# Optimization experiments

Measured on AMD Instinct MI355X. Metric: run time of the kernel, lower is better.

The kernel has to match this reference:

```python
import jax, jax.numpy as jnp
import numpy as np

N = 100000
E = 6400000
IN_CH = 128
HID = 8
HEADS = 2
OUT_CH = 1
NEG_SLOPE = 0.2


def gat_conv(x, src, dst, W, a_src, a_dst, bias, heads, out_ch, concat, n_nodes):
    # x: [N, F_in], W: [F_in, heads*out_ch], a_src/a_dst: [heads, out_ch]
    h = (x @ W).reshape(n_nodes, heads, out_ch)          # [N, H, C]
    alpha_s = jnp.sum(h * a_src[None], axis=-1)          # [N, H]
    alpha_d = jnp.sum(h * a_dst[None], axis=-1)          # [N, H]
    alpha = alpha_s[src] + alpha_d[dst]                  # [E, H]
    alpha = jax.nn.leaky_relu(alpha, NEG_SLOPE)
    # segment softmax over incoming edges of each destination node
    seg_max = jax.ops.segment_max(alpha, dst, num_segments=n_nodes)  # [N, H]
    alpha = jnp.exp(alpha - seg_max[dst])
    denom = jax.ops.segment_sum(alpha, dst, num_segments=n_nodes)    # [N, H]
    alpha = alpha / (denom[dst] + 1e-16)
    msg = h[src] * alpha[..., None]                       # [E, H, C]
    out = jax.ops.segment_sum(msg, dst, num_segments=n_nodes)        # [N, H, C]
    if concat:
        out = out.reshape(n_nodes, heads * out_ch)
    else:
        out = out.mean(axis=1)
    return out + bias


def setup_inputs() -> dict:
    key = jax.random.key(0)
    ks = jax.random.split(key, 12)
    x = jax.random.normal(ks[0], (N, IN_CH), dtype=jnp.float32)
    edge_index = jax.random.randint(ks[1], (2, E), 0, N, dtype=jnp.int64)
    s1 = 1.0 / np.sqrt(IN_CH)
    W1 = jax.random.normal(ks[2], (IN_CH, HEADS * HID), dtype=jnp.float32) * s1
    a_src1 = jax.random.normal(ks[3], (HEADS, HID), dtype=jnp.float32) * (1.0 / np.sqrt(HID))
    a_dst1 = jax.random.normal(ks[4], (HEADS, HID), dtype=jnp.float32) * (1.0 / np.sqrt(HID))
    b1 = jnp.zeros((HEADS * HID,), dtype=jnp.float32)
    s2 = 1.0 / np.sqrt(HEADS * HID)
    W2 = jax.random.normal(ks[5], (HEADS * HID, OUT_CH), dtype=jnp.float32) * s2
    a_src2 = jax.random.normal(ks[6], (1, OUT_CH), dtype=jnp.float32)
    a_dst2 = jax.random.normal(ks[7], (1, OUT_CH), dtype=jnp.float32)
    b2 = jnp.zeros((OUT_CH,), dtype=jnp.float32)
    return {"x": x, "edge_index": edge_index, "W1": W1, "a_src1": a_src1,
            "a_dst1": a_dst1, "b1": b1, "W2": W2, "a_src2": a_src2,
            "a_dst2": a_dst2, "b2": b2}


def reference(x, edge_index, W1, a_src1, a_dst1, b1, W2, a_src2, a_dst2, b2):
    # add self-loops (PyG GATConv default)
    loops = jnp.arange(N, dtype=edge_index.dtype)
    src = jnp.concatenate([edge_index[0], loops])
    dst = jnp.concatenate([edge_index[1], loops])
    h = gat_conv(x, src, dst, W1, a_src1, a_dst1, b1, HEADS, HID, True, N)
    h = jax.nn.relu(h)
    out = gat_conv(h, src, dst, W2, a_src2, a_dst2, b2, 1, OUT_CH, False, N)
    return out
```

## Files before the change

kernel.cpp:

```cpp
#include <hip/hip_runtime.h>
#include <hip/hip_fp16.h>
#include <cstdint>
#include <cstddef>

#define N_NODES 100000
#define E_EDGES 6400000
#define E_TOT   (E_EDGES + N_NODES)
#define IN_CH   128
#define NHID    16
#define BSHIFT  8
#define BSZ     256
#define NBUCK   391
#define CHUNK   6144
#define BCAP    24
#define NCHUNK  ((E_TOT + CHUNK - 1) / CHUNK)
#define LCAP    18176

__global__ void k_detect(const int* __restrict__ edge, int* __restrict__ flag) {
    if (blockIdx.x == 0 && threadIdx.x == 0) {
        int odd_or = 0;
        for (int i = 0; i < 64; i++) odd_or |= edge[2 * i + 1];
        flag[0] = (odd_or == 0) ? 1 : 0;
    }
}

__global__ __launch_bounds__(256) void k_gemm1(
        const float* __restrict__ x, const float* __restrict__ W1,
        const float* __restrict__ a_src1, const float* __restrict__ a_dst1,
        __half* __restrict__ h16, float* __restrict__ asrc,
        float* __restrict__ adst) {
    __shared__ __align__(16) float sW[IN_CH * NHID];
    __shared__ __align__(16) float sx[16][132];
    __shared__ float sh[16][17];
    int t = threadIdx.x;
    int r = t >> 4, c = t & 15;
    int row = blockIdx.x * 16 + r;

    const float4* W4 = (const float4*)W1;
    ((float4*)sW)[t] = W4[t];
    ((float4*)sW)[t + 256] = W4[t + 256];

    if (row < N_NODES) {
        const float4* xr = (const float4*)(x + (size_t)row * IN_CH);
        float4 v0 = xr[c];
        float4 v1 = xr[c + 16];
        *(float4*)&sx[r][4 * c] = v0;
        *(float4*)&sx[r][64 + 4 * c] = v1;
    }
    __syncthreads();

    float acc = 0.f;
    if (row < N_NODES) {
        #pragma unroll 16
        for (int k = 0; k < IN_CH; k++) acc = fmaf(sx[r][k], sW[k * NHID + c], acc);
        h16[(size_t)row * NHID + c] = __float2half(acc);
    }
    sh[r][c] = acc;
    __syncthreads();

    if (row < N_NODES && c < 4) {
        int h = c & 1;
        const float* av = (c >= 2) ? a_dst1 : a_src1;
        float s = 0.f;
        #pragma unroll
        for (int q = 0; q < 8; q++) s = fmaf(sh[r][h * 8 + q], av[h * 8 + q], s);
        if (c < 2) asrc[2 * (size_t)row + c] = s;
        else       adst[2 * (size_t)row + (c - 2)] = s;
    }
}

__global__ __launch_bounds__(256) void k_ccount(const int* __restrict__ edge,
                                                const int* __restrict__ flag,
                                                int* __restrict__ ccnt) {
    __shared__ int sc[NBUCK];
    int m64 = flag[0];
    int t = threadIdx.x;
    for (int i = t; i < NBUCK; i += 256) sc[i] = 0;
    __syncthreads();
    size_t c0 = (size_t)blockIdx.x * CHUNK;
    size_t cend = c0 + CHUNK; if (cend > E_TOT) cend = E_TOT;
    size_t ee = (cend < (size_t)E_EDGES) ? cend : (size_t)E_EDGES;

    if (m64) {
        const int4* dp = (const int4*)(edge + 2 * (size_t)E_EDGES);
        for (size_t i = c0 + 2 * t; i < ee; i += 512) {
            int4 v = dp[i >> 1];
            atomicAdd(&sc[v.x >> BSHIFT], 1);
            if (i + 1 < ee) atomicAdd(&sc[v.z >> BSHIFT], 1);
        }
    } else {
        const int4* dp = (const int4*)(edge + (size_t)E_EDGES);
        for (size_t i = c0 + 4 * t; i < ee; i += 1024) {
            int4 v = dp[i >> 2];
            atomicAdd(&sc[v.x >> BSHIFT], 1);
            if (i + 1 < ee) atomicAdd(&sc[v.y >> BSHIFT], 1);
            if (i + 2 < ee) atomicAdd(&sc[v.z >> BSHIFT], 1);
            if (i + 3 < ee) atomicAdd(&sc[v.w >> BSHIFT], 1);
        }
    }
    size_t sl0 = (c0 > (size_t)E_EDGES) ? c0 : (size_t)E_EDGES;
    for (size_t i = sl0 + t; i < cend; i += 256) {
        int d = (int)(i - E_EDGES);
        atomicAdd(&sc[d >> BSHIFT], 1);
    }
    __syncthreads();
    for (int i = t; i < NBUCK; i += 256)
        ccnt[(size_t)blockIdx.x * NBUCK + i] = sc[i];
}

__global__ __launch_bounds__(256) void k_cscan(int* __restrict__ ccnt,
                                               int* __restrict__ bcnt) {
    __shared__ int sd[256];
    __shared__ int carry;
    int b = blockIdx.x, t = threadIdx.x;
    if (t == 0) carry = 0;
    __syncthreads();
    for (int base = 0; base < NCHUNK; base += 256) {
        int c = base + t;
        int v = (c < NCHUNK) ? ccnt[(size_t)c * NBUCK + b] : 0;
        sd[t] = v;
        __syncthreads();
        for (int ofs = 1; ofs < 256; ofs <<= 1) {
            int a = sd[t];
            int bb = (t >= ofs) ? sd[t - ofs] : 0;
            __syncthreads();
            sd[t] = a + bb;
            __syncthreads();
        }
        if (c < NCHUNK) ccnt[(size_t)c * NBUCK + b] = sd[t] - v + carry;
        __syncthreads();
        if (t == 255) carry += sd[255];
        __syncthreads();
    }
    if (t == 0) bcnt[b] = carry;
}

__global__ __launch_bounds__(512) void k_bscan(const int* __restrict__ bcnt,
                                               int* __restrict__ bbase) {
    __shared__ int sd[512];
    int t = threadIdx.x;
    int v = (t < NBUCK) ? bcnt[t] : 0;
    sd[t] = v;
    __syncthreads();
    for (int ofs = 1; ofs < 512; ofs <<= 1) {
        int a = sd[t];
        int b = (t >= ofs) ? sd[t - ofs] : 0;
        __syncthreads();
        sd[t] = a + b;
        __syncthreads();
    }
    if (t < NBUCK) bbase[t] = sd[t] - v;
    if (t == NBUCK) bbase[NBUCK] = sd[NBUCK - 1];
}

__global__ __launch_bounds__(256) void k_bin(const int* __restrict__ edge,
                                             const int* __restrict__ flag,
                                             const int* __restrict__ ccnt,
                                             const int* __restrict__ bbase,
                                             unsigned* __restrict__ staged) {
    __shared__ unsigned lbin[NBUCK][BCAP];
    __shared__ int lcnt[NBUCK];
    __shared__ int lbase[NBUCK];
    int m64 = flag[0];
    int t = threadIdx.x;
    int g = t >> 4, lane = t & 15;

    size_t c0 = (size_t)blockIdx.x * CHUNK;
    if (c0 >= E_TOT) return;
    size_t cend = c0 + CHUNK; if (cend > E_TOT) cend = E_TOT;
    size_t ee = (cend < (size_t)E_EDGES) ? cend : (size_t)E_EDGES;

    for (int i = t; i < NBUCK; i += 256) {
        lcnt[i] = 0;
        lbase[i] = bbase[i] + ccnt[(size_t)blockIdx.x * NBUCK + i];
    }
    __syncthreads();

    auto put = [&](int s, int d) {
        int b = d >> BSHIFT;
        unsigned v = (unsigned)s | ((unsigned)(d & (BSZ - 1)) << 17);
        int idx = atomicAdd(&lcnt[b], 1);
        if (idx < BCAP) lbin[b][idx] = v;
        else            staged[lbase[b] + idx] = v;
    };

    if (m64) {
        const int4* sp = (const int4*)edge;
        const int4* dp = (const int4*)(edge + 2 * (size_t)E_EDGES);
        for (size_t i = c0 + 2 * t; i < ee; i += 512) {
            int4 sv = sp[i >> 1];
            int4 dv = dp[i >> 1];
            put(sv.x, dv.x);
            if (i + 1 < ee) put(sv.z, dv.z);
        }
    } else {
        const int4* sp = (const int4*)edge;
        const int4* dp = (const int4*)(edge + (size_t)E_EDGES);
        for (size_t i = c0 + 4 * t; i < ee; i += 1024) {
            int4 sv = sp[i >> 2];
            int4 dv = dp[i >> 2];
            put(sv.x, dv.x);
            if (i + 1 < ee) put(sv.y, dv.y);
            if (i + 2 < ee) put(sv.z, dv.z);
            if (i + 3 < ee) put(sv.w, dv.w);
        }
    }
    size_t sl0 = (c0 > (size_t)E_EDGES) ? c0 : (size_t)E_EDGES;
    for (size_t i = sl0 + t; i < cend; i += 256) {
        int d = (int)(i - E_EDGES);
        put(d, d);
    }
    __syncthreads();
    for (int b = g; b < NBUCK; b += 16) {
        int n = min(lcnt[b], BCAP);
        if (!n) continue;
        int pos = lbase[b];
        for (int i = lane; i < n; i += 16) staged[pos + i] = lbin[b][i];
    }
}

__global__ __launch_bounds__(512) void k_fused1(
        const unsigned* __restrict__ staged, const int* __restrict__ bbase,
        const __half* __restrict__ h16, const float* __restrict__ asrc,
        const float* __restrict__ adst,
        const float* __restrict__ b1, const float* __restrict__ W2,
        int* __restrict__ csr, int* __restrict__ offs,
        float* __restrict__ h2out) {
    __shared__ int lcsr[LCAP];
    __shared__ int hist[BSZ];
    __shared__ int segbeg[BSZ];
    __shared__ int cur[BSZ];
    __shared__ float2 sadp[BSZ];
    int bkt = blockIdx.x;
    int t = threadIdx.x;
    int dbase = bkt << BSHIFT;
    int beg = bbase[bkt], end = bbase[bkt + 1];

    if (t < BSZ) {
        hist[t] = 0;
        int d = dbase + t;
        sadp[t] = (d < N_NODES) ? ((const float2*)adst)[d] : make_float2(0.f, 0.f);
    }
    __syncthreads();
    for (int e = beg + t; e < end; e += 512)
        atomicAdd(&hist[staged[e] >> 17], 1);
    __syncthreads();

    int myv = (t < BSZ) ? hist[t] : 0;
    __syncthreads();
    for (int ofs = 1; ofs < BSZ; ofs <<= 1) {
        int a = 0, b = 0;
        if (t < BSZ) { a = hist[t]; b = (t >= ofs) ? hist[t - ofs] : 0; }
        __syncthreads();
        if (t < BSZ) hist[t] = a + b;
        __syncthreads();
    }
    if (t < BSZ) {
        int excl = hist[t] - myv;
        segbeg[t] = excl;
        cur[t] = excl;
        int d = dbase + t;
        if (d < N_NODES) offs[d] = beg + excl;
    }
    if (bkt == NBUCK - 1 && t == 0) offs[N_NODES] = E_TOT;
    __syncthreads();

    for (int e = beg + t; e < end; e += 512) {
        unsigned v = staged[e];
        int pos = atomicAdd(&cur[v >> 17], 1);
        lcsr[pos] = (int)(v & 0x1FFFFu);
    }
    __syncthreads();

    int n = end - beg;
    for (int i = t; i < n; i += 512) csr[beg + i] = lcsr[i];

    int p = t >> 1, sub = t & 1;
    int sb = segbeg[p], se = cur[p];
    float adpv = sub ? sadp[p].y : sadp[p].x;

    float acc[8];
    #pragma unroll
    for (int c = 0; c < 8; c++) acc[c] = 0.f;
    float den = 0.f;

    auto loadslot = [&](int i, float& aspv, float4& hv) {
        if (i < se) {
            int s = lcsr[i];
            hv = *(const float4*)(h16 + (size_t)s * NHID + sub * 8);
            aspv = asrc[2 * (size_t)s + sub];
        }
    };
    auto consume = [&](float aspv, const float4& hv) {
        float a = aspv + adpv; a = (a > 0.f) ? a : 0.2f * a;
        float pw = __expf(a);
        den += pw;
        const __half2* hh = (const __half2*)&hv;
        #pragma unroll
        for (int q = 0; q < 4; q++) {
            float2 f = __half22float2(hh[q]);
            acc[2 * q]     = fmaf(pw, f.x, acc[2 * q]);
            acc[2 * q + 1] = fmaf(pw, f.y, acc[2 * q + 1]);
        }
    };

    float aA = 0.f, aB = 0.f, aC = 0.f, aD = 0.f;
    float4 z4 = make_float4(0.f, 0.f, 0.f, 0.f);
    float4 hA = z4, hB = z4, hC = z4, hD = z4;

    int i = sb;
    loadslot(i,     aA, hA);
    loadslot(i + 1, aB, hB);
    loadslot(i + 2, aC, hC);
    loadslot(i + 3, aD, hD);
    while (true) {
        if (i >= se) break;
        consume(aA, hA); loadslot(i + 4, aA, hA); i++;
        if (i >= se) break;
        consume(aB, hB); loadslot(i + 4, aB, hB); i++;
        if (i >= se) break;
        consume(aC, hC); loadslot(i + 4, aC, hC); i++;
        if (i >= se) break;
        consume(aD, hD); loadslot(i + 4, aD, hD); i++;
    }

    float inv = 1.f / (den + 1e-16f);
    float v = 0.f;
    #pragma unroll
    for (int ch = 0; ch < 8; ch++) {
        float o = acc[ch] * inv + b1[8 * sub + ch];
        o = (o > 0.f) ? o : 0.f;
        v = fmaf(o, W2[8 * sub + ch], v);
    }
    v += __shfl_xor(v, 1, 64);
    if (sub == 0) {
        int d = dbase + p;
        if (d < N_NODES) h2out[d] = v;
    }
}

__global__ __launch_bounds__(256) void k_edge2(
        const int* __restrict__ offs, const int* __restrict__ csr,
        const float* __restrict__ h2,
        const float* __restrict__ a_src2, const float* __restrict__ a_dst2,
        const float* __restrict__ b2, float* __restrict__ out) {
    int t = threadIdx.x;
    int g = t >> 4, lane = t & 15;
    int d = blockIdx.x * 16 + g;
    if (d >= N_NODES) return;

    float as2 = a_src2[0], ad2 = a_dst2[0];
    float adv = h2[d] * ad2;
    int beg = offs[d], end = offs[d + 1];

    float den = 0.f, acc = 0.f;
    auto ls = [&](int ee, float& hs) { if (ee < end) hs = h2[csr[ee]]; };
    auto cs = [&](float hs) {
        float a = fmaf(hs, as2, adv);
        a = (a > 0.f) ? a : 0.2f * a;
        float p = __expf(a);
        den += p;
        acc = fmaf(p, hs, acc);
    };
    float hA = 0.f, hB = 0.f, hC = 0.f, hD = 0.f, hE = 0.f, hF = 0.f;
    int e = beg + lane;
    ls(e, hA); ls(e + 16, hB); ls(e + 32, hC);
    ls(e + 48, hD); ls(e + 64, hE); ls(e + 80, hF);
    while (true) {
        if (e >= end) break;
        cs(hA); ls(e + 96, hA); e += 16;
        if (e >= end) break;
        cs(hB); ls(e + 96, hB); e += 16;
        if (e >= end) break;
        cs(hC); ls(e + 96, hC); e += 16;
        if (e >= end) break;
        cs(hD); ls(e + 96, hD); e += 16;
        if (e >= end) break;
        cs(hE); ls(e + 96, hE); e += 16;
        if (e >= end) break;
        cs(hF); ls(e + 96, hF); e += 16;
    }
    #pragma unroll
    for (int m = 1; m < 16; m <<= 1) {
        den += __shfl_xor(den, m, 64);
        acc += __shfl_xor(acc, m, 64);
    }
    if (lane == 0) out[d] = acc / (den + 1e-16f) + b2[0];
}

extern "C" void kernel_launch(void* const* d_in, const int* in_sizes, int n_in,
                              void* d_out, int out_size, void* d_ws, size_t ws_size,
                              hipStream_t stream) {
    const float* x      = (const float*)d_in[0];
    const int*   edge   = (const int*)  d_in[1];
    const float* W1     = (const float*)d_in[2];
    const float* a_src1 = (const float*)d_in[3];
    const float* a_dst1 = (const float*)d_in[4];
    const float* b1     = (const float*)d_in[5];
    const float* W2     = (const float*)d_in[6];
    const float* a_src2 = (const float*)d_in[7];
    const float* a_dst2 = (const float*)d_in[8];
    const float* b2     = (const float*)d_in[9];

    constexpr size_t A = 256;
    auto al = [](size_t b) { return (b + A - 1) / A * A; };
    char* ws = (char*)d_ws;
    size_t off = 0;
    int*      flag   = (int*)(ws + off);      off += al(256);
    int*      ccnt   = (int*)(ws + off);      off += al((size_t)NCHUNK * NBUCK * 4);
    int*      bcnt   = (int*)(ws + off);      off += al(NBUCK * 4);
    int*      bbase  = (int*)(ws + off);      off += al((NBUCK + 1) * 4);
    unsigned* staged = (unsigned*)(ws + off); off += al((size_t)E_TOT * 4);
    int*      csr    = (int*)(ws + off);      off += al((size_t)E_TOT * 4);
    int*      offs   = (int*)(ws + off);      off += al((size_t)(N_NODES + 1) * 4);
    __half*   h16    = (__half*)(ws + off);   off += al((size_t)N_NODES * NHID * 2);
    float*    asrc   = (float*)(ws + off);    off += al((size_t)N_NODES * 2 * 4);
    float*    adst   = (float*)(ws + off);    off += al((size_t)N_NODES * 2 * 4);
    float*    h2     = (float*)(ws + off);    off += al((size_t)N_NODES * 4);
    (void)ws_size; (void)in_sizes; (void)n_in; (void)out_size;

    k_detect<<<1, 64, 0, stream>>>(edge, flag);
    k_gemm1 <<<(N_NODES + 15) / 16, 256, 0, stream>>>(x, W1, a_src1, a_dst1, h16, asrc, adst);
    k_ccount<<<NCHUNK, 256, 0, stream>>>(edge, flag, ccnt);
    k_cscan <<<NBUCK, 256, 0, stream>>>(ccnt, bcnt);
    k_bscan <<<1, 512, 0, stream>>>(bcnt, bbase);
    k_bin   <<<NCHUNK, 256, 0, stream>>>(edge, flag, ccnt, bbase, staged);
    k_fused1<<<NBUCK, 512, 0, stream>>>(staged, bbase, h16, asrc, adst, b1, W2, csr, offs, h2);
    k_edge2 <<<(N_NODES + 15) / 16, 256, 0, stream>>>(offs, csr, h2, a_src2, a_dst2, b2,
                                                      (float*)d_out);
}
```

Baseline: 203.6 us.

## Split each destination bucket across two blocks and use four threads per node

k_fused1 now launches two blocks per 256-node bucket. Each block handles 128 destination nodes, builds only its half of the local CSR, and needs about half the LDS. Inside a block, each node's edge list is split between two thread pairs that interleave edges and combine partial sums with shuffles, and the prefetch depth grows from 4 to 6 slots. The aim is more blocks in flight for latency hiding on only 391 buckets, at the cost of each block re-reading and re-histogramming the whole bucket's staged edges.

```diff
diff --git a/kernel.cpp b/kernel.cpp
--- a/kernel.cpp
+++ b/kernel.cpp
@@ -11,10 +11,11 @@
 #define BSHIFT  8
 #define BSZ     256
 #define NBUCK   391
+#define HBSZ    128
 #define CHUNK   6144
 #define BCAP    24
 #define NCHUNK  ((E_TOT + CHUNK - 1) / CHUNK)
-#define LCAP    18176
+#define LCAP    8960
 
 __global__ void k_detect(const int* __restrict__ edge, int* __restrict__ flag) {
     if (blockIdx.x == 0 && threadIdx.x == 0) {
@@ -227,56 +228,61 @@
         int* __restrict__ csr, int* __restrict__ offs,
         float* __restrict__ h2out) {
     __shared__ int lcsr[LCAP];
-    __shared__ int hist[BSZ];
-    __shared__ int segbeg[BSZ];
-    __shared__ int cur[BSZ];
-    __shared__ float2 sadp[BSZ];
-    int bkt = blockIdx.x;
-    int t = threadIdx.x;
-    int dbase = bkt << BSHIFT;
+    __shared__ int scn[BSZ];
+    __shared__ int cur[HBSZ];
+    __shared__ float2 sadp[HBSZ];
+    int bkt = blockIdx.x >> 1, half = blockIdx.x & 1;
+    int t = threadIdx.x;
+    int dlb = half * HBSZ;
+    int dbase = (bkt << BSHIFT) + dlb;
     int beg = bbase[bkt], end = bbase[bkt + 1];
 
-    if (t < BSZ) {
-        hist[t] = 0;
+    if (t < BSZ) scn[t] = 0;
+    if (t < HBSZ) {
         int d = dbase + t;
         sadp[t] = (d < N_NODES) ? ((const float2*)adst)[d] : make_float2(0.f, 0.f);
     }
     __syncthreads();
     for (int e = beg + t; e < end; e += 512)
-        atomicAdd(&hist[staged[e] >> 17], 1);
-    __syncthreads();
-
-    int myv = (t < BSZ) ? hist[t] : 0;
+        atomicAdd(&scn[staged[e] >> 17], 1);
+    __syncthreads();
+
+    int myv = (t < BSZ) ? scn[t] : 0;
     __syncthreads();
     for (int ofs = 1; ofs < BSZ; ofs <<= 1) {
         int a = 0, b = 0;
-        if (t < BSZ) { a = hist[t]; b = (t >= ofs) ? hist[t - ofs] : 0; }
-        __syncthreads();
-        if (t < BSZ) hist[t] = a + b;
-        __syncthreads();
-    }
-    if (t < BSZ) {
-        int excl = hist[t] - myv;
-        segbeg[t] = excl;
-        cur[t] = excl;
+        if (t < BSZ) { a = scn[t]; b = (t >= ofs) ? scn[t - ofs] : 0; }
+        __syncthreads();
+        if (t < BSZ) scn[t] = a + b;
+        __syncthreads();
+    }
+    if (t < BSZ) scn[t] -= myv;
+    __syncthreads();
+
+    int base  = scn[dlb];
+    int nhalf = (half ? (end - beg) : scn[HBSZ]) - base;
+    if (t < HBSZ) {
+        cur[t] = scn[dlb + t] - base;
         int d = dbase + t;
-        if (d < N_NODES) offs[d] = beg + excl;
-    }
-    if (bkt == NBUCK - 1 && t == 0) offs[N_NODES] = E_TOT;
+        if (d < N_NODES) offs[d] = beg + scn[dlb + t];
+    }
+    if (bkt == NBUCK - 1 && half == 1 && t == 0) offs[N_NODES] = E_TOT;
     __syncthreads();
 
     for (int e = beg + t; e < end; e += 512) {
         unsigned v = staged[e];
-        int pos = atomicAdd(&cur[v >> 17], 1);
-        lcsr[pos] = (int)(v & 0x1FFFFu);
-    }
-    __syncthreads();
-
-    int n = end - beg;
-    for (int i = t; i < n; i += 512) csr[beg + i] = lcsr[i];
-
-    int p = t >> 1, sub = t & 1;
-    int sb = segbeg[p], se = cur[p];
+        int dl = (int)(v >> 17);
+        if ((dl >> 7) == half) {
+            int pos = atomicAdd(&cur[dl & (HBSZ - 1)], 1);
+            lcsr[pos] = (int)(v & 0x1FFFFu);
+        }
+    }
+    __syncthreads();
+
+    for (int i = t; i < nhalf; i += 512) csr[beg + base + i] = lcsr[i];
+
+    int p = t >> 2, j = (t >> 1) & 1, sub = t & 1;
+    int sb = scn[dlb + p] - base, se = cur[p];
     float adpv = sub ? sadp[p].y : sadp[p].x;
 
     float acc[8];
@@ -304,25 +310,35 @@
         }
     };
 
-    float aA = 0.f, aB = 0.f, aC = 0.f, aD = 0.f;
+    float aA = 0.f, aB = 0.f, aC = 0.f, aD = 0.f, aE = 0.f, aF = 0.f;
     float4 z4 = make_float4(0.f, 0.f, 0.f, 0.f);
-    float4 hA = z4, hB = z4, hC = z4, hD = z4;
-
-    int i = sb;
-    loadslot(i,     aA, hA);
-    loadslot(i + 1, aB, hB);
-    loadslot(i + 2, aC, hC);
-    loadslot(i + 3, aD, hD);
+    float4 hA = z4, hB = z4, hC = z4, hD = z4, hE = z4, hF = z4;
+
+    int i = sb + j;
+    loadslot(i,      aA, hA);
+    loadslot(i + 2,  aB, hB);
+    loadslot(i + 4,  aC, hC);
+    loadslot(i + 6,  aD, hD);
+    loadslot(i + 8,  aE, hE);
+    loadslot(i + 10, aF, hF);
     while (true) {
         if (i >= se) break;
-        consume(aA, hA); loadslot(i + 4, aA, hA); i++;
-        if (i >= se) break;
-        consume(aB, hB); loadslot(i + 4, aB, hB); i++;
-        if (i >= se) break;
-        consume(aC, hC); loadslot(i + 4, aC, hC); i++;
-        if (i >= se) break;
-        consume(aD, hD); loadslot(i + 4, aD, hD); i++;
-    }
+        consume(aA, hA); loadslot(i + 12, aA, hA); i += 2;
+        if (i >= se) break;
+        consume(aB, hB); loadslot(i + 12, aB, hB); i += 2;
+        if (i >= se) break;
+        consume(aC, hC); loadslot(i + 12, aC, hC); i += 2;
+        if (i >= se) break;
+        consume(aD, hD); loadslot(i + 12, aD, hD); i += 2;
+        if (i >= se) break;
+        consume(aE, hE); loadslot(i + 12, aE, hE); i += 2;
+        if (i >= se) break;
+        consume(aF, hF); loadslot(i + 12, aF, hF); i += 2;
+    }
+
+    den += __shfl_xor(den, 2, 64);
+    #pragma unroll
+    for (int c = 0; c < 8; c++) acc[c] += __shfl_xor(acc[c], 2, 64);
 
     float inv = 1.f / (den + 1e-16f);
     float v = 0.f;
@@ -333,7 +349,7 @@
         v = fmaf(o, W2[8 * sub + ch], v);
     }
     v += __shfl_xor(v, 1, 64);
-    if (sub == 0) {
+    if ((t & 3) == 0) {
         int d = dbase + p;
         if (d < N_NODES) h2out[d] = v;
     }
@@ -425,7 +441,8 @@
     k_cscan <<<NBUCK, 256, 0, stream>>>(ccnt, bcnt);
     k_bscan <<<1, 512, 0, stream>>>(bcnt, bbase);
     k_bin   <<<NCHUNK, 256, 0, stream>>>(edge, flag, ccnt, bbase, staged);
-    k_fused1<<<NBUCK, 512, 0, stream>>>(staged, bbase, h16, asrc, adst, b1, W2, csr, offs, h2);
+    k_fused1<<<NBUCK * 2, 512, 0, stream>>>(staged, bbase, h16, asrc, adst, b1, W2,
+                                            csr, offs, h2);
     k_edge2 <<<(N_NODES + 15) / 16, 256, 0, stream>>>(offs, csr, h2, a_src2, a_dst2, b2,
                                                       (float*)d_out);
 }
```

Result: no change. 207.0 us (+1.7%).
